# Kernel tuning notes

Hardware: AMD Instinct MI355X
Metric: run time of the kernel (lower is better)

Reference implementation:

```python
import jax, jax.numpy as jnp
import numpy as np

MARGIN = 1.0
EPS = 1e-08


def setup_inputs() -> dict:
    key = jax.random.key(0)
    k0, k1 = jax.random.split(key)
    kernels0 = jax.random.normal(k0, (2048, 3, 3), dtype=jnp.float32)
    kernels1 = jax.random.normal(k1, (1024, 5, 5), dtype=jnp.float32)
    return {"kernels0": kernels0, "kernels1": kernels1}


def _layer_loss(kernels):
    n, d, _ = kernels.shape
    # Frobenius-normalize each kernel
    norms = jnp.sqrt(jnp.sum(kernels * kernels, axis=(1, 2), keepdims=True)) + EPS
    kn = kernels / norms                      # (n, d, d)
    inv = jnp.linalg.inv(kn)                  # (n, d, d)
    # AB[i, j] = inv[i] @ kn[j]; BA[i, j] = inv[j] @ kn[i]
    ab = jnp.einsum('iab,jbc->ijac', inv, kn)  # (n, n, d, d)
    ba = jnp.einsum('jab,ibc->ijac', inv, kn)  # (n, n, d, d)
    eye = jnp.eye(d, dtype=kernels.dtype)
    diff_ab = jnp.sqrt(jnp.sum((eye - ab) ** 2, axis=(2, 3)))  # (n, n)
    diff_ba = jnp.sqrt(jnp.sum((eye - ba) ** 2, axis=(2, 3)))  # (n, n)
    combined = jnp.tril(diff_ab) + jnp.triu(diff_ba)
    loss_mat = jax.nn.relu(MARGIN - combined)
    mask = ~jnp.eye(n, dtype=bool)
    loss_mat = jnp.where(mask, loss_mat, 0.0)
    return jnp.sum(loss_mat) / (n * (n - 1))


def reference(kernels0, kernels1):
    losses = [_layer_loss(kernels0), _layer_loss(kernels1)]
    return sum(losses) / len(losses)
```

## Files before the change

kernel.cpp:

```cpp
#include <hip/hip_runtime.h>
#include <math.h>

#define N0 2048
#define N1 1024
#define M0T 32
#define M1T 32
#define NB0 (M0T * (M0T + 1) / 2)
#define NB1 (M1T * (M1T + 1) / 2)
#define NBTOT (NB0 + NB1)


__device__ __forceinline__ void tri_decode(int t, int& bi, int& bj) {
    int b = (int)((sqrtf(8.0f * t + 1.0f) - 1.0f) * 0.5f);
    while ((b + 1) * (b + 2) / 2 <= t) ++b;
    while (b * (b + 1) / 2 > t) --b;
    bi = b;
    bj = t - b * (b + 1) / 2;
}

__device__ __forceinline__ void inv3_to(const float* __restrict__ g, float* __restrict__ dst) {
    float a[9];
    float ss = 0.0f;
#pragma unroll
    for (int e = 0; e < 9; ++e) { a[e] = g[e]; ss = fmaf(a[e], a[e], ss); }
    float rn = 1.0f / (sqrtf(ss) + 1e-8f);
#pragma unroll
    for (int e = 0; e < 9; ++e) a[e] *= rn;
    float c00 = a[4] * a[8] - a[5] * a[7];
    float c01 = -(a[3] * a[8] - a[5] * a[6]);
    float c02 = a[3] * a[7] - a[4] * a[6];
    float det = a[0] * c00 + a[1] * c01 + a[2] * c02;
    float id = 1.0f / det;
    float x[9];
    x[0] = c00 * id;
    x[1] = (a[2] * a[7] - a[1] * a[8]) * id;
    x[2] = (a[1] * a[5] - a[2] * a[4]) * id;
    x[3] = c01 * id;
    x[4] = (a[0] * a[8] - a[2] * a[6]) * id;
    x[5] = (a[2] * a[3] - a[0] * a[5]) * id;
    x[6] = c02 * id;
    x[7] = (a[1] * a[6] - a[0] * a[7]) * id;
    x[8] = (a[0] * a[4] - a[1] * a[3]) * id;
    float r[9];
#pragma unroll
    for (int i = 0; i < 3; ++i)
#pragma unroll
        for (int j = 0; j < 3; ++j) {
            float m = a[i * 3 + 0] * x[0 * 3 + j];
            m = fmaf(a[i * 3 + 1], x[1 * 3 + j], m);
            m = fmaf(a[i * 3 + 2], x[2 * 3 + j], m);
            r[i * 3 + j] = ((i == j) ? 2.0f : 0.0f) - m;
        }
#pragma unroll
    for (int i = 0; i < 3; ++i)
#pragma unroll
        for (int j = 0; j < 3; ++j) {
            float m = x[i * 3 + 0] * r[0 * 3 + j];
            m = fmaf(x[i * 3 + 1], r[1 * 3 + j], m);
            m = fmaf(x[i * 3 + 2], r[2 * 3 + j], m);
            dst[i * 3 + j] = m;
        }
}

__device__ __forceinline__ void norm3_to(const float* __restrict__ g, float* __restrict__ dst) {
    float a[9];
    float ss = 0.0f;
#pragma unroll
    for (int e = 0; e < 9; ++e) { a[e] = g[e]; ss = fmaf(a[e], a[e], ss); }
    float rn = 1.0f / (sqrtf(ss) + 1e-8f);
#pragma unroll
    for (int e = 0; e < 9; ++e) dst[e] = a[e] * rn;
}

__device__ __forceinline__ void inv5_to(const float* __restrict__ g, float* __restrict__ dst) {
    float A[5][5], B[5][5];
    float ss = 0.0f;
#pragma unroll
    for (int r = 0; r < 5; ++r)
#pragma unroll
        for (int c = 0; c < 5; ++c) {
            float v = g[r * 5 + c];
            A[r][c] = v;
            ss = fmaf(v, v, ss);
        }
    float rn = 1.0f / (sqrtf(ss) + 1e-8f);
#pragma unroll
    for (int r = 0; r < 5; ++r)
#pragma unroll
        for (int c = 0; c < 5; ++c) {
            A[r][c] *= rn;
            B[r][c] = (r == c) ? 1.0f : 0.0f;
        }
#pragma unroll
    for (int k = 0; k < 5; ++k) {
#pragma unroll
        for (int r = k + 1; r < 5; ++r) {
            bool sw = fabsf(A[r][k]) > fabsf(A[k][k]);
#pragma unroll
            for (int c = k; c < 5; ++c) {
                float Ar = A[r][c], Ak = A[k][c];
                A[r][c] = sw ? Ak : Ar;
                A[k][c] = sw ? Ar : Ak;
            }
#pragma unroll
            for (int c = 0; c < 5; ++c) {
                float Br = B[r][c], Bk = B[k][c];
                B[r][c] = sw ? Bk : Br;
                B[k][c] = sw ? Br : Bk;
            }
        }
        float piv = 1.0f / A[k][k];
#pragma unroll
        for (int c = k; c < 5; ++c) A[k][c] *= piv;
#pragma unroll
        for (int c = 0; c < 5; ++c) B[k][c] *= piv;
#pragma unroll
        for (int r = 0; r < 5; ++r) {
            if (r == k) continue;
            float f = A[r][k];
#pragma unroll
            for (int c = k; c < 5; ++c) A[r][c] = fmaf(-f, A[k][c], A[r][c]);
#pragma unroll
            for (int c = 0; c < 5; ++c) B[r][c] = fmaf(-f, B[k][c], B[r][c]);
        }
    }
#pragma unroll
    for (int r = 0; r < 5; ++r)
#pragma unroll
        for (int c = 0; c < 5; ++c) dst[r * 5 + c] = B[r][c];
}

__device__ __forceinline__ void norm5_to(const float* __restrict__ g, float* __restrict__ dst) {
    float a[25];
    float ss = 0.0f;
#pragma unroll
    for (int e = 0; e < 25; ++e) { a[e] = g[e]; ss = fmaf(a[e], a[e], ss); }
    float rn = 1.0f / (sqrtf(ss) + 1e-8f);
#pragma unroll
    for (int e = 0; e < 25; ++e) dst[e] = a[e] * rn;
}

__global__ __launch_bounds__(256, 4) void pairs_kernel(const float* __restrict__ k0,
                                                       const float* __restrict__ k1,
                                                       float* __restrict__ partial) {
    __shared__ __align__(16) float sA[896];
    __shared__ __align__(16) float sB[896];
    int tid = threadIdx.x;
    float contrib = 0.0f;

    if (blockIdx.x < NB0) {
        int bi, bj;
        tri_decode(blockIdx.x, bi, bj);

        if (tid < 64) {
            inv3_to(k0 + (bi * 64 + tid) * 9, sA + tid * 12);
        } else if (tid < 128) {
            int j = tid - 64;
            norm3_to(k0 + (bj * 64 + j) * 9, sB + j * 12);
        }
        __syncthreads();

        int ti = tid >> 4, tj = tid & 15;
        int ibase = bi * 64 + ti * 4, jbase = bj * 64 + tj * 4;
        float a[4][12];
#pragma unroll
        for (int u = 0; u < 4; ++u) {
            float4* d = (float4*)a[u];
            const float4* s = (const float4*)(sA + (ti * 4 + u) * 12);
            d[0] = s[0]; d[1] = s[1]; d[2] = s[2];
        }
        __builtin_amdgcn_sched_barrier(0);
#pragma unroll
        for (int v = 0; v < 4; ++v) {
            float b[12];
            {
                float4* d = (float4*)b;
                const float4* s = (const float4*)(sB + (tj * 4 + v) * 12);
                d[0] = s[0]; d[1] = s[1]; d[2] = s[2];
            }
#pragma unroll
            for (int u = 0; u < 4; ++u) {
                float s = 0.0f;
#pragma unroll
                for (int r = 0; r < 3; ++r)
#pragma unroll
                    for (int c = 0; c < 3; ++c) {
                        float m = a[u][r * 3 + 0] * b[c];
                        m = fmaf(a[u][r * 3 + 1], b[3 + c], m);
                        m = fmaf(a[u][r * 3 + 2], b[6 + c], m);
                        float d = ((r == c) ? 1.0f : 0.0f) - m;
                        s = fmaf(d, d, s);
                    }
                bool take = ((ibase + u) > (jbase + v)) && (s < 1.0f);
                contrib += take ? (1.0f - __builtin_amdgcn_sqrtf(s)) : 0.0f;
            }
        }
    } else {
        int bi, bj;
        tri_decode(blockIdx.x - NB0, bi, bj);

        if (tid < 32) {
            inv5_to(k1 + (bi * 32 + tid) * 25, sA + tid * 28);
        } else if (tid < 64) {
            int j = tid - 32;
            norm5_to(k1 + (bj * 32 + j) * 25, sB + j * 28);
        }
        __syncthreads();

        int ti = tid >> 4, tj = tid & 15;
        int ibase = bi * 32 + ti * 2, jbase = bj * 32 + tj * 2;
        float a[2][28];
#pragma unroll
        for (int u = 0; u < 2; ++u) {
            float4* d = (float4*)a[u];
            const float4* s = (const float4*)(sA + (ti * 2 + u) * 28);
#pragma unroll
            for (int q = 0; q < 7; ++q) d[q] = s[q];
        }
        __builtin_amdgcn_sched_barrier(0);
#pragma unroll
        for (int v = 0; v < 2; ++v) {
            float b[28];
            {
                float4* d = (float4*)b;
                const float4* s = (const float4*)(sB + (tj * 2 + v) * 28);
#pragma unroll
                for (int q = 0; q < 7; ++q) d[q] = s[q];
            }
#pragma unroll
            for (int u = 0; u < 2; ++u) {
                float s = 0.0f;
#pragma unroll
                for (int r = 0; r < 5; ++r)
#pragma unroll
                    for (int c = 0; c < 5; ++c) {
                        float m = a[u][r * 5 + 0] * b[c];
#pragma unroll
                        for (int k = 1; k < 5; ++k) m = fmaf(a[u][r * 5 + k], b[k * 5 + c], m);
                        float d = ((r == c) ? 1.0f : 0.0f) - m;
                        s = fmaf(d, d, s);
                    }
                bool take = ((ibase + u) > (jbase + v)) && (s < 1.0f);
                contrib += take ? (1.0f - __builtin_amdgcn_sqrtf(s)) : 0.0f;
            }
        }
    }

#pragma unroll
    for (int off = 32; off; off >>= 1) contrib += __shfl_down(contrib, off);
    __shared__ float wsum[4];
    if ((tid & 63) == 0) wsum[tid >> 6] = contrib;
    __syncthreads();
    if (tid == 0) partial[blockIdx.x] = wsum[0] + wsum[1] + wsum[2] + wsum[3];
}

__global__ void finalize_kernel(const float* __restrict__ partial, float* __restrict__ out) {
    int tid = threadIdx.x;
    double s0 = 0.0, s1 = 0.0;
    for (int x = tid; x < NB0; x += 256) s0 += (double)partial[x];
    for (int x = NB0 + tid; x < NBTOT; x += 256) s1 += (double)partial[x];
#pragma unroll
    for (int off = 32; off; off >>= 1) {
        s0 += __shfl_down(s0, off);
        s1 += __shfl_down(s1, off);
    }
    __shared__ double w0[4], w1[4];
    if ((tid & 63) == 0) { w0[tid >> 6] = s0; w1[tid >> 6] = s1; }
    __syncthreads();
    if (tid == 0) {
        double S0 = w0[0] + w0[1] + w0[2] + w0[3];
        double S1 = w1[0] + w1[1] + w1[2] + w1[3];
        double res = S0 / ((double)N0 * (double)(N0 - 1)) +
                     S1 / ((double)N1 * (double)(N1 - 1));
        out[0] = (float)res;
    }
}

extern "C" void kernel_launch(void* const* d_in, const int* in_sizes, int n_in,
                              void* d_out, int out_size, void* d_ws, size_t ws_size,
                              hipStream_t stream) {
    const float* k0 = (const float*)d_in[0];
    const float* k1 = (const float*)d_in[1];
    float* out = (float*)d_out;

    float* partial = (float*)d_ws;

    pairs_kernel<<<NBTOT, 256, 0, stream>>>(k0, k1, partial);
    finalize_kernel<<<1, 256, 0, stream>>>(partial, out);
}
```

Baseline: 65.01 us.

## Pair adjacent column tiles per block to halve block count and reuse inverses

Each block now covers two adjacent column tiles of the lower triangle instead of one, so the per-row-tile inverse computation is amortized over twice the pairs. The grid shrinks from 1056 to 544 blocks, with a new triangular decode over paired columns. The inner column loop becomes runtime-bounded and is no longer unrolled. That can cost instruction scheduling, and fewer blocks may underfill the GPU's compute units.

```diff
diff --git a/kernel.cpp b/kernel.cpp
--- a/kernel.cpp
+++ b/kernel.cpp
@@ -5,17 +5,20 @@
 #define N1 1024
 #define M0T 32
 #define M1T 32
-#define NB0 (M0T * (M0T + 1) / 2)
-#define NB1 (M1T * (M1T + 1) / 2)
-#define NBTOT (NB0 + NB1)
-
-
-__device__ __forceinline__ void tri_decode(int t, int& bi, int& bj) {
-    int b = (int)((sqrtf(8.0f * t + 1.0f) - 1.0f) * 0.5f);
-    while ((b + 1) * (b + 2) / 2 <= t) ++b;
-    while (b * (b + 1) / 2 > t) --b;
+#define NBP 272
+#define NBTOTP (2 * NBP)
+
+
+__device__ __forceinline__ int pbase(int bi) {
+    return (bi & 1) ? (((bi + 1) >> 1) * ((bi + 1) >> 1)) : ((bi * (bi + 2)) >> 2);
+}
+__device__ __forceinline__ void ptri_decode(int p, int& bi, int& bjp) {
+    int b = (int)(2.0f * sqrtf((float)p + 0.25f));
+    if (b > M0T - 1) b = M0T - 1;
+    while (b + 1 <= M0T - 1 && pbase(b + 1) <= p) ++b;
+    while (pbase(b) > p) --b;
     bi = b;
-    bj = t - b * (b + 1) / 2;
+    bjp = p - pbase(b);
 }
 
 __device__ __forceinline__ void inv3_to(const float* __restrict__ g, float* __restrict__ dst) {
@@ -144,24 +147,29 @@
                                                        const float* __restrict__ k1,
                                                        float* __restrict__ partial) {
     __shared__ __align__(16) float sA[896];
-    __shared__ __align__(16) float sB[896];
+    __shared__ __align__(16) float sB[1792];
     int tid = threadIdx.x;
     float contrib = 0.0f;
 
-    if (blockIdx.x < NB0) {
-        int bi, bj;
-        tri_decode(blockIdx.x, bi, bj);
+    if (blockIdx.x < NBP) {
+        int bi, bjp;
+        ptri_decode(blockIdx.x, bi, bjp);
+        int bj2 = 2 * bjp;
+        int jc = (bj2 + 1 <= bi) ? 2 : 1;
+        int ncol = 64 * jc;
 
         if (tid < 64) {
             inv3_to(k0 + (bi * 64 + tid) * 9, sA + tid * 12);
-        } else if (tid < 128) {
+        } else if (tid < 64 + ncol) {
             int j = tid - 64;
-            norm3_to(k0 + (bj * 64 + j) * 9, sB + j * 12);
+            norm3_to(k0 + ((bj2 * 64) + j) * 9, sB + j * 12);
         }
         __syncthreads();
 
         int ti = tid >> 4, tj = tid & 15;
-        int ibase = bi * 64 + ti * 4, jbase = bj * 64 + tj * 4;
+        int ibase = bi * 64 + ti * 4;
+        int cols_per = 4 * jc;
+        int jbase = bj2 * 64 + tj * cols_per;
         float a[4][12];
 #pragma unroll
         for (int u = 0; u < 4; ++u) {
@@ -170,12 +178,12 @@
             d[0] = s[0]; d[1] = s[1]; d[2] = s[2];
         }
         __builtin_amdgcn_sched_barrier(0);
-#pragma unroll
-        for (int v = 0; v < 4; ++v) {
+        for (int v = 0; v < cols_per; ++v) {
+            int col = tj * cols_per + v;
             float b[12];
             {
                 float4* d = (float4*)b;
-                const float4* s = (const float4*)(sB + (tj * 4 + v) * 12);
+                const float4* s = (const float4*)(sB + col * 12);
                 d[0] = s[0]; d[1] = s[1]; d[2] = s[2];
             }
 #pragma unroll
@@ -184,11 +192,11 @@
 #pragma unroll
                 for (int r = 0; r < 3; ++r)
 #pragma unroll
-                    for (int c = 0; c < 3; ++c) {
-                        float m = a[u][r * 3 + 0] * b[c];
-                        m = fmaf(a[u][r * 3 + 1], b[3 + c], m);
-                        m = fmaf(a[u][r * 3 + 2], b[6 + c], m);
-                        float d = ((r == c) ? 1.0f : 0.0f) - m;
+                    for (int cc = 0; cc < 3; ++cc) {
+                        float m = a[u][r * 3 + 0] * b[cc];
+                        m = fmaf(a[u][r * 3 + 1], b[3 + cc], m);
+                        m = fmaf(a[u][r * 3 + 2], b[6 + cc], m);
+                        float d = ((r == cc) ? 1.0f : 0.0f) - m;
                         s = fmaf(d, d, s);
                     }
                 bool take = ((ibase + u) > (jbase + v)) && (s < 1.0f);
@@ -196,19 +204,24 @@
             }
         }
     } else {
-        int bi, bj;
-        tri_decode(blockIdx.x - NB0, bi, bj);
+        int bi, bjp;
+        ptri_decode(blockIdx.x - NBP, bi, bjp);
+        int bj2 = 2 * bjp;
+        int jc = (bj2 + 1 <= bi) ? 2 : 1;
+        int ncol = 32 * jc;
 
         if (tid < 32) {
             inv5_to(k1 + (bi * 32 + tid) * 25, sA + tid * 28);
-        } else if (tid < 64) {
-            int j = tid - 32;
-            norm5_to(k1 + (bj * 32 + j) * 25, sB + j * 28);
+        } else if (tid >= 64 && tid < 64 + ncol) {
+            int j = tid - 64;
+            norm5_to(k1 + ((bj2 * 32) + j) * 25, sB + j * 28);
         }
         __syncthreads();
 
         int ti = tid >> 4, tj = tid & 15;
-        int ibase = bi * 32 + ti * 2, jbase = bj * 32 + tj * 2;
+        int ibase = bi * 32 + ti * 2;
+        int cols_per = 2 * jc;
+        int jbase = bj2 * 32 + tj * cols_per;
         float a[2][28];
 #pragma unroll
         for (int u = 0; u < 2; ++u) {
@@ -218,12 +231,12 @@
             for (int q = 0; q < 7; ++q) d[q] = s[q];
         }
         __builtin_amdgcn_sched_barrier(0);
-#pragma unroll
-        for (int v = 0; v < 2; ++v) {
+        for (int v = 0; v < cols_per; ++v) {
+            int col = tj * cols_per + v;
             float b[28];
             {
                 float4* d = (float4*)b;
-                const float4* s = (const float4*)(sB + (tj * 2 + v) * 28);
+                const float4* s = (const float4*)(sB + col * 28);
 #pragma unroll
                 for (int q = 0; q < 7; ++q) d[q] = s[q];
             }
@@ -233,11 +246,11 @@
 #pragma unroll
                 for (int r = 0; r < 5; ++r)
 #pragma unroll
-                    for (int c = 0; c < 5; ++c) {
-                        float m = a[u][r * 5 + 0] * b[c];
-#pragma unroll
-                        for (int k = 1; k < 5; ++k) m = fmaf(a[u][r * 5 + k], b[k * 5 + c], m);
-                        float d = ((r == c) ? 1.0f : 0.0f) - m;
+                    for (int cc = 0; cc < 5; ++cc) {
+                        float m = a[u][r * 5 + 0] * b[cc];
+#pragma unroll
+                        for (int k = 1; k < 5; ++k) m = fmaf(a[u][r * 5 + k], b[k * 5 + cc], m);
+                        float d = ((r == cc) ? 1.0f : 0.0f) - m;
                         s = fmaf(d, d, s);
                     }
                 bool take = ((ibase + u) > (jbase + v)) && (s < 1.0f);
@@ -257,8 +270,8 @@
 __global__ void finalize_kernel(const float* __restrict__ partial, float* __restrict__ out) {
     int tid = threadIdx.x;
     double s0 = 0.0, s1 = 0.0;
-    for (int x = tid; x < NB0; x += 256) s0 += (double)partial[x];
-    for (int x = NB0 + tid; x < NBTOT; x += 256) s1 += (double)partial[x];
+    for (int x = tid; x < NBP; x += 256) s0 += (double)partial[x];
+    for (int x = NBP + tid; x < NBTOTP; x += 256) s1 += (double)partial[x];
 #pragma unroll
     for (int off = 32; off; off >>= 1) {
         s0 += __shfl_down(s0, off);
@@ -285,6 +298,6 @@
 
     float* partial = (float*)d_ws;
 
-    pairs_kernel<<<NBTOT, 256, 0, stream>>>(k0, k1, partial);
+    pairs_kernel<<<NBTOTP, 256, 0, stream>>>(k0, k1, partial);
     finalize_kernel<<<1, 256, 0, stream>>>(partial, out);
 }
```

Measured after the change: 65.46 us. Within noise of the previous version (+0.7%).
